# Kernel optimization log

Measured on AMD Instinct MI355X. Metric: run time of the kernel, lower is better.

The kernel has to match this reference:

```python
import jax, jax.numpy as jnp
import numpy as np

N = 8192
F_IN = 1024
F_OUT = 512

def glorot(key, shape):
    limit = np.sqrt(6.0 / (shape[0] + shape[1]))
    return jax.random.uniform(key, shape, minval=-limit, maxval=limit, dtype=jnp.float32)

def setup_inputs() -> dict:
    key = jax.random.key(0)
    k1, k2, k3 = jax.random.split(key, 3)
    x = jax.random.normal(k1, (N, F_IN), dtype=jnp.float32)
    adj = jax.random.uniform(k2, (N, N), dtype=jnp.float32)  # dense nonnegative adjacency
    W = glorot(k3, (F_IN, F_OUT))
    b = jnp.zeros((F_OUT,), dtype=jnp.float32)
    return {"x": x, "adj": adj, "W": W, "b": b}

def reference(x, adj, W, b):
    # GCN layer: relu( D^{-1/2} (A + I) D^{-1/2} @ (x @ W) + b )
    n = adj.shape[0]
    A = adj + jnp.eye(n, dtype=adj.dtype)            # add self loops (tf.diag(In))
    d = jnp.sum(A, axis=1)                            # row-sum degrees
    d_is = d ** -0.5                                  # D^{-1/2}
    # D1 @ A @ D1 expressed as row/col scaling (identical math, no diag GEMMs)
    A_norm = A * d_is[:, None] * d_is[None, :]
    pre_sup = x @ W                                   # [N, F_OUT]
    out = A_norm @ pre_sup + b                        # propagation + bias
    return jax.nn.relu(out)
```

## Files before the change

kernel.cpp:

```cpp
#include <hip/hip_runtime.h>
#include <stdint.h>

#define NN 8192
#define FIN 1024
#define FOUT 512

typedef __attribute__((ext_vector_type(4))) float f32x4;
typedef __attribute__((ext_vector_type(8))) short s16x8;
typedef __attribute__((ext_vector_type(4))) unsigned short u16x4;

__device__ __forceinline__ short f2bf(float f) {
    return __builtin_bit_cast(short, static_cast<__bf16>(f));
}
__device__ __forceinline__ float bf2f(short s) {
    return (float)__builtin_bit_cast(__bf16, s);
}

__global__ __launch_bounds__(256) void prep_kernel(const float* __restrict__ adj,
                                                   short* __restrict__ adjB,
                                                   float* __restrict__ d_is,
                                                   const float* __restrict__ x,
                                                   short* __restrict__ xB,
                                                   const float* __restrict__ W,
                                                   short* __restrict__ WT) {
    __shared__ float red[4];
    __shared__ float T[64][68];
    const int b = blockIdx.x;
    const int t = threadIdx.x;
    if (b < NN) {
        const int row = b;
        const float4* a = reinterpret_cast<const float4*>(adj + (size_t)row * NN);
        u16x4* ob = reinterpret_cast<u16x4*>(adjB + (size_t)row * NN);
        float s = 0.f;
        #pragma unroll 2
        for (int j = t; j < NN / 4; j += 256) {
            float4 v = a[j];
            s += (v.x + v.y) + (v.z + v.w);
            u16x4 p;
            p[0] = (unsigned short)f2bf(v.x); p[1] = (unsigned short)f2bf(v.y);
            p[2] = (unsigned short)f2bf(v.z); p[3] = (unsigned short)f2bf(v.w);
            ob[j] = p;
        }
        #pragma unroll
        for (int off = 32; off > 0; off >>= 1) s += __shfl_down(s, off, 64);
        if ((t & 63) == 0) red[t >> 6] = s;
        __syncthreads();
        if (t == 0) {
            const float d = red[0] + red[1] + red[2] + red[3] + 1.0f;
            d_is[row] = 1.0f / sqrtf(d);
        }
    } else if (b < NN + 4096) {
        const size_t i = ((size_t)(b - NN) * 256 + t) * 8;
        const float4 v0 = *reinterpret_cast<const float4*>(&x[i]);
        const float4 v1 = *reinterpret_cast<const float4*>(&x[i + 4]);
        s16x8 o;
        o[0] = f2bf(v0.x); o[1] = f2bf(v0.y); o[2] = f2bf(v0.z); o[3] = f2bf(v0.w);
        o[4] = f2bf(v1.x); o[5] = f2bf(v1.y); o[6] = f2bf(v1.z); o[7] = f2bf(v1.w);
        *reinterpret_cast<s16x8*>(&xB[i]) = o;
    } else {
        const int bid = b - NN - 4096;
        const int wc = bid & 7;
        const int wk = bid >> 3;
        const int cc = (t & 15) * 4;
        #pragma unroll
        for (int i = 0; i < 4; ++i) {
            const int rr = (t >> 4) + i * 16;
            *reinterpret_cast<float4*>(&T[rr][cc]) =
                *reinterpret_cast<const float4*>(&W[(size_t)(wk * 64 + rr) * FOUT + wc * 64 + cc]);
        }
        __syncthreads();
        const int a = t >> 2;
        const int b0 = (t & 3) * 16;
        s16x8 v0, v1;
        #pragma unroll
        for (int e = 0; e < 8; ++e) { v0[e] = f2bf(T[b0 + e][a]); v1[e] = f2bf(T[b0 + 8 + e][a]); }
        short* dst = &WT[(size_t)(wc * 64 + a) * FIN + wk * 64 + b0];
        *reinterpret_cast<s16x8*>(dst) = v0;
        *reinterpret_cast<s16x8*>(dst + 8) = v1;
    }
}

__global__ __launch_bounds__(256) void rowsum_kernel(const float* __restrict__ adj,
                                                     float* __restrict__ d_is) {
    const int row = blockIdx.x;
    const float4* a = reinterpret_cast<const float4*>(adj + (size_t)row * NN);
    float s = 0.f;
    #pragma unroll 4
    for (int j = threadIdx.x; j < NN / 4; j += 256) {
        float4 v = a[j];
        s += (v.x + v.y) + (v.z + v.w);
    }
    #pragma unroll
    for (int off = 32; off > 0; off >>= 1) s += __shfl_down(s, off, 64);
    __shared__ float red[4];
    if ((threadIdx.x & 63) == 0) red[threadIdx.x >> 6] = s;
    __syncthreads();
    if (threadIdx.x == 0) {
        const float d = red[0] + red[1] + red[2] + red[3] + 1.0f;
        d_is[row] = 1.0f / sqrtf(d);
    }
}

__global__ __launch_bounds__(256) void wt_kernel(const float* __restrict__ W,
                                                 short* __restrict__ WT) {
    __shared__ float T[64][68];
    const int wc = blockIdx.x;
    const int wk = blockIdx.y;
    const int t = threadIdx.x;
    const int cc = (t & 15) * 4;
    #pragma unroll
    for (int i = 0; i < 4; ++i) {
        const int rr = (t >> 4) + i * 16;
        *reinterpret_cast<float4*>(&T[rr][cc]) =
            *reinterpret_cast<const float4*>(&W[(size_t)(wk * 64 + rr) * FOUT + wc * 64 + cc]);
    }
    __syncthreads();
    const int a = t >> 2;
    const int b0 = (t & 3) * 16;
    s16x8 v0, v1;
    #pragma unroll
    for (int e = 0; e < 8; ++e) { v0[e] = f2bf(T[b0 + e][a]); v1[e] = f2bf(T[b0 + 8 + e][a]); }
    short* dst = &WT[(size_t)(wc * 64 + a) * FIN + wk * 64 + b0];
    *reinterpret_cast<s16x8*>(dst) = v0;
    *reinterpret_cast<s16x8*>(dst + 8) = v1;
}

__global__ __launch_bounds__(256, 4) void xwg_kernel(const short* __restrict__ xB,
                                                     const short* __restrict__ WT,
                                                     const float* __restrict__ d_is,
                                                     short* __restrict__ psT) {
    constexpr int NT = FIN / 32;
    __shared__ short As[2][4096];
    __shared__ short Bs[2][2048];

    const int tid = threadIdx.x;
    const int lin = blockIdx.x;
    const int swz = (lin & 7) * 64 + (lin >> 3);
    const int col0 = (swz & 7) * 64;
    const int row0 = (swz >> 3) * 128;

    const int lane = tid & 63;
    const int wv = tid >> 6;
    const int wr = wv >> 1, wc = wv & 1;
    const int l15 = lane & 15;
    const int kq = lane >> 4;
    const int xorv = (l15 & 12) << 2;

    int arow[2], acoff[2];
    #pragma unroll
    for (int i = 0; i < 2; ++i) {
        const int slot = i * 256 + tid;
        const int P = (slot << 4) ^ (slot & 48);
        arow[i] = P >> 6;
        acoff[i] = (P & 63) >> 1;
    }
    const short* Ab = xB + (size_t)row0 * FIN;
    const short* Bb = WT + (size_t)col0 * FIN;

    auto stage = [&](int buf, int k0) {
        #pragma unroll
        for (int i = 0; i < 2; ++i) {
            const short* src = Ab + (size_t)arow[i] * FIN + k0 + acoff[i];
            short* dst = &As[buf][(i * 256 + (tid & 192)) * 8];
            __builtin_amdgcn_global_load_lds(
                (const __attribute__((address_space(1))) unsigned int*)src,
                (__attribute__((address_space(3))) unsigned int*)dst, 16, 0, 0);
        }
        {
            const short* src = Bb + (size_t)arow[0] * FIN + k0 + acoff[0];
            short* dst = &Bs[buf][(tid & 192) * 8];
            __builtin_amdgcn_global_load_lds(
                (const __attribute__((address_space(1))) unsigned int*)src,
                (__attribute__((address_space(3))) unsigned int*)dst, 16, 0, 0);
        }
    };

    f32x4 acc[4][2] = {};
    auto compute = [&](int buf) {
        s16x8 af[4], bfr[2];
        #pragma unroll
        for (int m = 0; m < 4; ++m) {
            const int byteoff = ((wr * 64 + m * 16 + l15) * 64 + kq * 16) ^ xorv;
            af[m] = *reinterpret_cast<const s16x8*>(&As[buf][byteoff >> 1]);
        }
        #pragma unroll
        for (int n = 0; n < 2; ++n) {
            const int byteoff = ((wc * 32 + n * 16 + l15) * 64 + kq * 16) ^ xorv;
            bfr[n] = *reinterpret_cast<const s16x8*>(&Bs[buf][byteoff >> 1]);
        }
        #pragma unroll
        for (int m = 0; m < 4; ++m)
            #pragma unroll
            for (int n = 0; n < 2; ++n)
                acc[m][n] = __builtin_amdgcn_mfma_f32_16x16x32_bf16(af[m], bfr[n], acc[m][n], 0, 0, 0);
    };

    stage(0, 0);
    stage(1, 32);
    int cur = 0;
    #pragma unroll 1
    for (int t = 0; t < NT; ++t) {
        if (t < NT - 1) {
            asm volatile("s_waitcnt vmcnt(3)" ::: "memory");
        } else {
            asm volatile("s_waitcnt vmcnt(0)" ::: "memory");
        }
        __builtin_amdgcn_s_barrier();
        compute(cur);
        if (t + 2 < NT) {
            __builtin_amdgcn_s_barrier();
            stage(cur, (t + 2) * 32);
        }
        cur ^= 1;
    }

    #pragma unroll
    for (int m = 0; m < 4; ++m) {
        const int rbase = row0 + wr * 64 + m * 16 + kq * 4;
        float dr[4];
        #pragma unroll
        for (int j = 0; j < 4; ++j) dr[j] = d_is[rbase + j];
        #pragma unroll
        for (int n = 0; n < 2; ++n) {
            const int col = col0 + wc * 32 + n * 16 + l15;
            u16x4 pk;
            #pragma unroll
            for (int j = 0; j < 4; ++j) pk[j] = (unsigned short)f2bf(dr[j] * acc[m][n][j]);
            *reinterpret_cast<u16x4*>(&psT[(size_t)col * NN + rbase]) = pk;
        }
    }
}

__global__ __launch_bounds__(512, 1) void prop3_kernel(
    const short* __restrict__ adjB, const short* __restrict__ psT,
    short* __restrict__ Pb0, short* __restrict__ Pb1,
    short* __restrict__ Pb2, short* __restrict__ Pb3) {
    extern __shared__ short L[];

    const int tid = threadIdx.x;
    const int lin = blockIdx.x;
    const int swz = (lin & 7) * 32 + (lin >> 3);
    const int col0 = (swz & 1) * 256;
    const int ks = (swz >> 1) & 3;
    const int row0 = (swz >> 3) * 256;

    const int lane = tid & 63;
    const int wv = tid >> 6;
    const int wr = wv >> 2;
    const int wc = wv & 3;
    const int l15 = lane & 15;
    const int kq = lane >> 4;
    const int xorv = (l15 & 12) << 2;

    int srow[2], scol[2];
    #pragma unroll
    for (int i = 0; i < 2; ++i) {
        const int slot = i * 512 + tid;
        const int P = (slot << 4) ^ (slot & 48);
        srow[i] = P >> 6;
        scol[i] = (P & 63) >> 1;
    }
    const size_t kbase = (size_t)ks * 2048;
    const short* Ab = adjB + (size_t)row0 * NN + kbase;
    const short* Bb = psT + (size_t)col0 * NN + kbase;

    auto stageH = [&](int buf, int op, int kh, int t) {
        const short* s0 = op ? Bb : Ab;
        const int k0 = t * 64 + kh * 32;
        short* base = &L[buf * 32768 + op * 16384 + kh * 8192];
        #pragma unroll
        for (int i = 0; i < 2; ++i) {
            const short* src = s0 + (size_t)srow[i] * NN + k0 + scol[i];
            short* dst = base + (i * 512 + (tid & 448)) * 8;
            __builtin_amdgcn_global_load_lds(
                (const __attribute__((address_space(1))) unsigned int*)src,
                (__attribute__((address_space(3))) unsigned int*)dst, 16, 0, 0);
        }
    };

    f32x4 acc[8][4] = {};

#define LDFRAG(BASE, ROW) \
    (*reinterpret_cast<const s16x8*>(&(BASE)[((((ROW) * 64 + kq * 16)) ^ xorv) >> 1]))

#define PHASE(BUF, KH, QM, STAGE_STMT, VM_STMT)                                     \
    do {                                                                            \
        const short* Ah_ = &L[(BUF) * 32768 + (KH) * 8192];                         \
        const short* Bh_ = &L[(BUF) * 32768 + 16384 + (KH) * 8192];                 \
        s16x8 af_[4], bg_[4];                                                       \
        _Pragma("unroll")                                                           \
        for (int m = 0; m < 4; ++m)                                                 \
            af_[m] = LDFRAG(Ah_, wr * 128 + (QM) * 64 + m * 16 + l15);              \
        _Pragma("unroll")                                                           \
        for (int n = 0; n < 4; ++n)                                                 \
            bg_[n] = LDFRAG(Bh_, wc * 64 + n * 16 + l15);                           \
        STAGE_STMT;                                                                 \
        asm volatile("" ::: "memory");                                              \
        __builtin_amdgcn_s_barrier();                                               \
        __builtin_amdgcn_s_setprio(1);                                              \
        _Pragma("unroll")                                                           \
        for (int m = 0; m < 4; ++m)                                                 \
            _Pragma("unroll")                                                       \
            for (int n = 0; n < 4; ++n)                                             \
                acc[(QM) * 4 + m][n] = __builtin_amdgcn_mfma_f32_16x16x32_bf16(     \
                    af_[m], bg_[n], acc[(QM) * 4 + m][n], 0, 0, 0);                 \
        __builtin_amdgcn_s_setprio(0);                                              \
        VM_STMT;                                                                    \
        asm volatile("" ::: "memory");                                              \
        __builtin_amdgcn_s_barrier();                                               \
    } while (0)

#define VM4 asm volatile("s_waitcnt vmcnt(4)" ::: "memory")
#define VM0 asm volatile("s_waitcnt vmcnt(0)" ::: "memory")

    stageH(0, 0, 0, 0); stageH(0, 1, 0, 0);
    stageH(0, 0, 1, 0); stageH(0, 1, 1, 0);
    stageH(1, 0, 0, 1); stageH(1, 1, 0, 1);
    asm volatile("s_waitcnt vmcnt(8)" ::: "memory");
    __builtin_amdgcn_s_barrier();

    PHASE(0, 0, 0, (void)0,             (void)0);
    PHASE(0, 0, 1, (void)0,             VM4);
    PHASE(0, 1, 0, stageH(1, 0, 1, 1),  (void)0);
    PHASE(0, 1, 1, stageH(1, 1, 1, 1),  VM4);

    #pragma unroll 1
    for (int t = 1; t <= 30; ++t) {
        const int buf = t & 1, nb = buf ^ 1, tn = t + 1;
        PHASE(buf, 0, 0, stageH(nb, 0, 0, tn), (void)0);
        PHASE(buf, 0, 1, stageH(nb, 1, 0, tn), VM4);
        PHASE(buf, 1, 0, stageH(nb, 0, 1, tn), (void)0);
        PHASE(buf, 1, 1, stageH(nb, 1, 1, tn), VM4);
    }

    PHASE(1, 0, 0, (void)0, (void)0);
    PHASE(1, 0, 1, (void)0, VM0);
    PHASE(1, 1, 0, (void)0, (void)0);
    PHASE(1, 1, 1, (void)0, (void)0);

    {
        short* Pt = (ks == 0) ? Pb0 : (ks == 1) ? Pb1 : (ks == 2) ? Pb2 : Pb3;
        #pragma unroll
        for (int mi = 0; mi < 8; ++mi) {
            const int rbase = row0 + wr * 128 + mi * 16 + kq * 4;
            #pragma unroll
            for (int n = 0; n < 4; ++n) {
                const int col = col0 + wc * 64 + n * 16 + l15;
                #pragma unroll
                for (int j = 0; j < 4; ++j)
                    Pt[(size_t)(rbase + j) * FOUT + col] = f2bf(acc[mi][n][j]);
            }
        }
    }
#undef PHASE
#undef LDFRAG
#undef VM4
#undef VM0
}

__global__ __launch_bounds__(256) void ep4_kernel(
    const short* __restrict__ Pb0, const short* __restrict__ Pb1,
    const short* __restrict__ Pb2, const short* __restrict__ Pb3,
    float* __restrict__ out,
    const short* __restrict__ psT, const float* __restrict__ d_is,
    const float* __restrict__ bias) {
    const int col0 = blockIdx.x * 128;
    const int row0 = blockIdx.y * 32;
    const int t = threadIdx.x;
    const int c = col0 + (t & 31) * 4;
    const float4 bb = *reinterpret_cast<const float4*>(&bias[c]);
    #pragma unroll
    for (int it = 0; it < 4; ++it) {
        const int r = row0 + (t >> 5) + it * 8;
        const size_t idx = (size_t)r * FOUT + c;
        const u16x4 a = *reinterpret_cast<const u16x4*>(&Pb0[idx]);
        const u16x4 b4 = *reinterpret_cast<const u16x4*>(&Pb1[idx]);
        const u16x4 c4 = *reinterpret_cast<const u16x4*>(&Pb2[idx]);
        const u16x4 d4 = *reinterpret_cast<const u16x4*>(&Pb3[idx]);
        const float dr = d_is[r];
        float s[4], o4[4];
        #pragma unroll
        for (int j = 0; j < 4; ++j) s[j] = bf2f(psT[(size_t)(c + j) * NN + r]);
        const float bbv[4] = {bb.x, bb.y, bb.z, bb.w};
        #pragma unroll
        for (int j = 0; j < 4; ++j) {
            const float sum = ((bf2f((short)a[j]) + bf2f((short)b4[j])) +
                               (bf2f((short)c4[j]) + bf2f((short)d4[j]))) + s[j];
            o4[j] = fmaxf(dr * sum + bbv[j], 0.f);
        }
        float4 o = {o4[0], o4[1], o4[2], o4[3]};
        *reinterpret_cast<float4*>(&out[idx]) = o;
    }
}

template<int KLEN, int MODE>
__global__ __launch_bounds__(256, 4) void gemm_kernel(
    const float* __restrict__ A, const short* __restrict__ B,
    const float* __restrict__ d_is,
    short* __restrict__ psT,
    float* __restrict__ P0, float* __restrict__ P1) {
    constexpr int KS = (MODE == 1) ? 2 : 1;
    constexpr int Ksub = KLEN / KS;
    constexpr int NT = Ksub / 32;
    constexpr int LDA = 40;
    __shared__ short As[2][128 * LDA];
    __shared__ short Bs[2][64 * LDA];

    const int tid = threadIdx.x;
    const int nchunk = gridDim.x >> 3;
    const int lin = blockIdx.x;
    const int swz = (lin & 7) * nchunk + (lin >> 3);
    const int col0 = (swz & 7) * 64;
    const int yp = (swz >> 3) & 63;
    const int ks = swz >> 9;
    const int row0 = yp * 128;
    const int kbase = ks * Ksub;

    const int lane = tid & 63;
    const int wv = tid >> 6;
    const int wr = wv >> 1, wc = wv & 1;
    const int l15 = lane & 15;
    const int koff = (lane >> 4) * 8;

    const int ar = tid >> 1, ak = (tid & 1) * 16;
    const float* Abase = A + (size_t)(row0 + ar) * KLEN + kbase + ak;
    const int br = tid >> 2, bk = (tid & 3) * 8;
    const short* Bbase = B + (size_t)(col0 + br) * KLEN + kbase + bk;

    float4 qa0, qa1, qa2, qa3;
    s16x8 qb;
    auto loadG = [&](int k0) {
        const float4* p = reinterpret_cast<const float4*>(Abase + k0);
        qa0 = p[0]; qa1 = p[1]; qa2 = p[2]; qa3 = p[3];
        qb = *reinterpret_cast<const s16x8*>(Bbase + k0);
    };
    auto writeL = [&](int buf) {
        const float a[16] = {qa0.x, qa0.y, qa0.z, qa0.w, qa1.x, qa1.y, qa1.z, qa1.w,
                             qa2.x, qa2.y, qa2.z, qa2.w, qa3.x, qa3.y, qa3.z, qa3.w};
        s16x8 v0, v1;
        #pragma unroll
        for (int e = 0; e < 8; ++e) { v0[e] = f2bf(a[e]); v1[e] = f2bf(a[8 + e]); }
        *reinterpret_cast<s16x8*>(&As[buf][ar * LDA + ak]) = v0;
        *reinterpret_cast<s16x8*>(&As[buf][ar * LDA + ak + 8]) = v1;
        *reinterpret_cast<s16x8*>(&Bs[buf][br * LDA + bk]) = qb;
    };

    f32x4 acc[4][2] = {};
    auto compute = [&](int buf) {
        s16x8 af[4], bfr[2];
        #pragma unroll
        for (int m = 0; m < 4; ++m)
            af[m] = *reinterpret_cast<const s16x8*>(&As[buf][(wr * 64 + m * 16 + l15) * LDA + koff]);
        #pragma unroll
        for (int n = 0; n < 2; ++n)
            bfr[n] = *reinterpret_cast<const s16x8*>(&Bs[buf][(wc * 32 + n * 16 + l15) * LDA + koff]);
        #pragma unroll
        for (int m = 0; m < 4; ++m)
            #pragma unroll
            for (int n = 0; n < 2; ++n)
                acc[m][n] = __builtin_amdgcn_mfma_f32_16x16x32_bf16(af[m], bfr[n], acc[m][n], 0, 0, 0);
    };

    loadG(0);
    writeL(0);
    __syncthreads();
    int cur = 0;
    for (int t = 0; t < NT; ++t) {
        if (t + 1 < NT) loadG((t + 1) * 32);
        compute(cur);
        if (t + 1 < NT) writeL(cur ^ 1);
        __syncthreads();
        cur ^= 1;
    }

    if (MODE == 0) {
        #pragma unroll
        for (int m = 0; m < 4; ++m) {
            const int rbase = row0 + wr * 64 + m * 16 + (lane >> 4) * 4;
            float dr[4];
            #pragma unroll
            for (int j = 0; j < 4; ++j) dr[j] = d_is[rbase + j];
            #pragma unroll
            for (int n = 0; n < 2; ++n) {
                const int col = col0 + wc * 32 + n * 16 + l15;
                u16x4 pk;
                #pragma unroll
                for (int j = 0; j < 4; ++j) pk[j] = (unsigned short)f2bf(dr[j] * acc[m][n][j]);
                *reinterpret_cast<u16x4*>(&psT[(size_t)col * NN + rbase]) = pk;
            }
        }
    } else {
        float* tgt = (ks == 0) ? P0 : P1;
        #pragma unroll
        for (int m = 0; m < 4; ++m) {
            const int rbase = row0 + wr * 64 + m * 16 + (lane >> 4) * 4;
            #pragma unroll
            for (int n = 0; n < 2; ++n) {
                const int col = col0 + wc * 32 + n * 16 + l15;
                f32x4 v = acc[m][n];
                if (ks == 0) {
                    const u16x4 sv = *reinterpret_cast<const u16x4*>(&psT[(size_t)col * NN + rbase]);
                    #pragma unroll
                    for (int j = 0; j < 4; ++j) v[j] += bf2f((short)sv[j]);
                }
                #pragma unroll
                for (int j = 0; j < 4; ++j)
                    tgt[(size_t)(rbase + j) * FOUT + col] = v[j];
            }
        }
    }
}

__global__ __launch_bounds__(256) void ep_kernel(const float* __restrict__ P0,
                                                 float* __restrict__ out,
                                                 const float* __restrict__ d_is,
                                                 const float* __restrict__ bias) {
    const size_t idx = ((size_t)blockIdx.x * 256 + threadIdx.x) * 4;
    const int row = (int)(idx >> 9);
    const int col = (int)(idx & 511);
    const float4 p0 = *reinterpret_cast<const float4*>(&P0[idx]);
    const float4 p1 = *reinterpret_cast<const float4*>(&out[idx]);
    const float4 bb = *reinterpret_cast<const float4*>(&bias[col]);
    const float dr = d_is[row];
    float4 o;
    o.x = fmaxf(dr * (p0.x + p1.x) + bb.x, 0.f);
    o.y = fmaxf(dr * (p0.y + p1.y) + bb.y, 0.f);
    o.z = fmaxf(dr * (p0.z + p1.z) + bb.z, 0.f);
    o.w = fmaxf(dr * (p0.w + p1.w) + bb.w, 0.f);
    *reinterpret_cast<float4*>(&out[idx]) = o;
}

extern "C" void kernel_launch(void* const* d_in, const int* in_sizes, int n_in,
                              void* d_out, int out_size, void* d_ws, size_t ws_size,
                              hipStream_t stream) {
    const float* x   = (const float*)d_in[0];
    const float* adj = (const float*)d_in[1];
    const float* W   = (const float*)d_in[2];
    const float* b   = (const float*)d_in[3];
    float* out = (float*)d_out;

    const size_t NEED = (size_t)FOUT * NN * 2 + (size_t)FOUT * FIN * 2
                      + (size_t)NN * FIN * 2 + 4ull * NN * FOUT * 2
                      + NN * 4 + (size_t)NN * NN * 2;

    if (ws_size >= NEED) {
        short* psT = (short*)d_ws;
        short* WT  = psT + (size_t)FOUT * NN;
        short* xB  = WT + (size_t)FOUT * FIN;
        short* Pb0 = xB + (size_t)NN * FIN;
        short* Pb1 = Pb0 + (size_t)NN * FOUT;
        short* Pb2 = Pb1 + (size_t)NN * FOUT;
        short* Pb3 = Pb2 + (size_t)NN * FOUT;
        float* dis = (float*)(Pb3 + (size_t)NN * FOUT);
        short* adjB = (short*)(dis + NN);

        hipLaunchKernelGGL(prep_kernel, dim3(NN + 4096 + 128), dim3(256), 0, stream,
                           adj, adjB, dis, x, xB, W, WT);
        hipLaunchKernelGGL(xwg_kernel, dim3(512), dim3(256), 0, stream, xB, WT, dis, psT);
        hipLaunchKernelGGL(prop3_kernel, dim3(256), dim3(512), 131072, stream,
                           adjB, psT, Pb0, Pb1, Pb2, Pb3);
        hipLaunchKernelGGL(ep4_kernel, dim3(4, 256), dim3(256), 0, stream,
                           Pb0, Pb1, Pb2, Pb3, out, psT, dis, b);
    } else {
        short* psT = (short*)d_ws;
        short* WT  = psT + (size_t)FOUT * NN;
        float* P0  = (float*)(WT + (size_t)FOUT * FIN);
        float* dis = P0 + (size_t)NN * FOUT;

        hipLaunchKernelGGL(rowsum_kernel, dim3(NN), dim3(256), 0, stream, adj, dis);
        hipLaunchKernelGGL(wt_kernel, dim3(8, 16), dim3(256), 0, stream, W, WT);
        hipLaunchKernelGGL((gemm_kernel<FIN, 0>), dim3(512), dim3(256), 0, stream,
                           x, WT, dis, psT, nullptr, nullptr);
        hipLaunchKernelGGL((gemm_kernel<NN, 1>), dim3(1024), dim3(256), 0, stream,
                           adj, psT, dis, psT, P0, out);
        hipLaunchKernelGGL(ep_kernel, dim3(NN * FOUT / 1024), dim3(256), 0, stream,
                           P0, out, dis, b);
    }
}
```

Measured before the change: 192.1 us.

## Convert fp32 adjacency to bf16 inside propagation GEMM instead of materializing adjB

After: 244.5 us. 1.27x slower.

```diff
diff --git a/kernel.cpp b/kernel.cpp
--- a/kernel.cpp
+++ b/kernel.cpp
@@ -17,7 +17,6 @@
 }
 
 __global__ __launch_bounds__(256) void prep_kernel(const float* __restrict__ adj,
-                                                   short* __restrict__ adjB,
                                                    float* __restrict__ d_is,
                                                    const float* __restrict__ x,
                                                    short* __restrict__ xB,
@@ -30,16 +29,11 @@
     if (b < NN) {
         const int row = b;
         const float4* a = reinterpret_cast<const float4*>(adj + (size_t)row * NN);
-        u16x4* ob = reinterpret_cast<u16x4*>(adjB + (size_t)row * NN);
         float s = 0.f;
-        #pragma unroll 2
+        #pragma unroll 4
         for (int j = t; j < NN / 4; j += 256) {
             float4 v = a[j];
             s += (v.x + v.y) + (v.z + v.w);
-            u16x4 p;
-            p[0] = (unsigned short)f2bf(v.x); p[1] = (unsigned short)f2bf(v.y);
-            p[2] = (unsigned short)f2bf(v.z); p[3] = (unsigned short)f2bf(v.w);
-            ob[j] = p;
         }
         #pragma unroll
         for (int off = 32; off > 0; off >>= 1) s += __shfl_down(s, off, 64);
@@ -231,8 +225,8 @@
     }
 }
 
-__global__ __launch_bounds__(512, 1) void prop3_kernel(
-    const short* __restrict__ adjB, const short* __restrict__ psT,
+__global__ __launch_bounds__(512, 1) void prop4_kernel(
+    const float* __restrict__ adj, const short* __restrict__ psT,
     short* __restrict__ Pb0, short* __restrict__ Pb1,
     short* __restrict__ Pb2, short* __restrict__ Pb3) {
     extern __shared__ short L[];
@@ -261,20 +255,44 @@
         scol[i] = (P & 63) >> 1;
     }
     const size_t kbase = (size_t)ks * 2048;
-    const short* Ab = adjB + (size_t)row0 * NN + kbase;
     const short* Bb = psT + (size_t)col0 * NN + kbase;
 
-    auto stageH = [&](int buf, int op, int kh, int t) {
-        const short* s0 = op ? Bb : Ab;
+    auto stageB = [&](int buf, int kh, int t) {
         const int k0 = t * 64 + kh * 32;
-        short* base = &L[buf * 32768 + op * 16384 + kh * 8192];
+        short* base = &L[buf * 32768 + 16384 + kh * 8192];
         #pragma unroll
         for (int i = 0; i < 2; ++i) {
-            const short* src = s0 + (size_t)srow[i] * NN + k0 + scol[i];
+            const short* src = Bb + (size_t)srow[i] * NN + k0 + scol[i];
             short* dst = base + (i * 512 + (tid & 448)) * 8;
             __builtin_amdgcn_global_load_lds(
                 (const __attribute__((address_space(1))) unsigned int*)src,
                 (__attribute__((address_space(3))) unsigned int*)dst, 16, 0, 0);
+        }
+    };
+
+    const int ar = tid & 255;
+    const int akh = tid >> 8;
+    const float* Abase = adj + (size_t)(row0 + ar) * NN + kbase + akh * 32;
+    const int axr = (ar >> 2) & 3;
+    float4 qa0, qa1, qa2, qa3, qa4, qa5, qa6, qa7;
+
+    auto loadA = [&](int t) {
+        const float4* p = reinterpret_cast<const float4*>(Abase + t * 64);
+        qa0 = p[0]; qa1 = p[1]; qa2 = p[2]; qa3 = p[3];
+        qa4 = p[4]; qa5 = p[5]; qa6 = p[6]; qa7 = p[7];
+    };
+    auto writeA = [&](int buf) {
+        short* base = &L[buf * 32768 + akh * 8192 + ar * 32];
+        const float fa[32] = {qa0.x, qa0.y, qa0.z, qa0.w, qa1.x, qa1.y, qa1.z, qa1.w,
+                              qa2.x, qa2.y, qa2.z, qa2.w, qa3.x, qa3.y, qa3.z, qa3.w,
+                              qa4.x, qa4.y, qa4.z, qa4.w, qa5.x, qa5.y, qa5.z, qa5.w,
+                              qa6.x, qa6.y, qa6.z, qa6.w, qa7.x, qa7.y, qa7.z, qa7.w};
+        #pragma unroll
+        for (int c = 0; c < 4; ++c) {
+            s16x8 v;
+            #pragma unroll
+            for (int e = 0; e < 8; ++e) v[e] = f2bf(fa[c * 8 + e]);
+            *reinterpret_cast<s16x8*>(base + (c ^ axr) * 8) = v;
         }
     };
 
@@ -310,27 +328,37 @@
         __builtin_amdgcn_s_barrier();                                               \
     } while (0)
 
-#define VM4 asm volatile("s_waitcnt vmcnt(4)" ::: "memory")
-#define VM0 asm volatile("s_waitcnt vmcnt(0)" ::: "memory")
-
-    stageH(0, 0, 0, 0); stageH(0, 1, 0, 0);
-    stageH(0, 0, 1, 0); stageH(0, 1, 1, 0);
-    stageH(1, 0, 0, 1); stageH(1, 1, 0, 1);
-    asm volatile("s_waitcnt vmcnt(8)" ::: "memory");
+#define WRITEA(NB)                                                                  \
+    do { writeA(NB);                                                                \
+         asm volatile("s_waitcnt lgkmcnt(0)" ::: "memory");                         \
+         __builtin_amdgcn_sched_barrier(0); } while (0)
+
+#define VM10 asm volatile("s_waitcnt vmcnt(10)" ::: "memory")
+#define VM2  asm volatile("s_waitcnt vmcnt(2)" ::: "memory")
+#define VM0  asm volatile("s_waitcnt vmcnt(0)" ::: "memory")
+
+    loadA(0);
+    writeA(0);
+    asm volatile("s_waitcnt lgkmcnt(0)" ::: "memory");
+    __builtin_amdgcn_sched_barrier(0);
+    stageB(0, 0, 0); stageB(0, 1, 0);
+    loadA(1);
+    stageB(1, 0, 1);
+    asm volatile("s_waitcnt vmcnt(12)" ::: "memory");
     __builtin_amdgcn_s_barrier();
 
-    PHASE(0, 0, 0, (void)0,             (void)0);
-    PHASE(0, 0, 1, (void)0,             VM4);
-    PHASE(0, 1, 0, stageH(1, 0, 1, 1),  (void)0);
-    PHASE(0, 1, 1, stageH(1, 1, 1, 1),  VM4);
+    PHASE(0, 0, 0, (void)0,           (void)0);
+    PHASE(0, 0, 1, (void)0,           VM10);
+    PHASE(0, 1, 0, WRITEA(1),         (void)0);
+    PHASE(0, 1, 1, stageB(1, 1, 1),   VM2);
 
     #pragma unroll 1
     for (int t = 1; t <= 30; ++t) {
         const int buf = t & 1, nb = buf ^ 1, tn = t + 1;
-        PHASE(buf, 0, 0, stageH(nb, 0, 0, tn), (void)0);
-        PHASE(buf, 0, 1, stageH(nb, 1, 0, tn), VM4);
-        PHASE(buf, 1, 0, stageH(nb, 0, 1, tn), (void)0);
-        PHASE(buf, 1, 1, stageH(nb, 1, 1, tn), VM4);
+        PHASE(buf, 0, 0, loadA(tn),           (void)0);
+        PHASE(buf, 0, 1, stageB(nb, 0, tn),   VM10);
+        PHASE(buf, 1, 0, WRITEA(nb),          (void)0);
+        PHASE(buf, 1, 1, stageB(nb, 1, tn),   VM2);
     }
 
     PHASE(1, 0, 0, (void)0, (void)0);
@@ -338,24 +366,25 @@
     PHASE(1, 1, 0, (void)0, (void)0);
     PHASE(1, 1, 1, (void)0, (void)0);
 
-    {
-        short* Pt = (ks == 0) ? Pb0 : (ks == 1) ? Pb1 : (ks == 2) ? Pb2 : Pb3;
-        #pragma unroll
-        for (int mi = 0; mi < 8; ++mi) {
-            const int rbase = row0 + wr * 128 + mi * 16 + kq * 4;
-            #pragma unroll
-            for (int n = 0; n < 4; ++n) {
-                const int col = col0 + wc * 64 + n * 16 + l15;
-                #pragma unroll
-                for (int j = 0; j < 4; ++j)
-                    Pt[(size_t)(rbase + j) * FOUT + col] = f2bf(acc[mi][n][j]);
-            }
-        }
-    }
 #undef PHASE
 #undef LDFRAG
-#undef VM4
+#undef WRITEA
+#undef VM10
+#undef VM2
 #undef VM0
+
+    short* Pt = (ks == 0) ? Pb0 : (ks == 1) ? Pb1 : (ks == 2) ? Pb2 : Pb3;
+    #pragma unroll
+    for (int mi = 0; mi < 8; ++mi) {
+        const int rbase = row0 + wr * 128 + mi * 16 + kq * 4;
+        #pragma unroll
+        for (int n = 0; n < 4; ++n) {
+            const int col = col0 + wc * 64 + n * 16 + l15;
+            #pragma unroll
+            for (int j = 0; j < 4; ++j)
+                Pt[(size_t)(rbase + j) * FOUT + col] = f2bf(acc[mi][n][j]);
+        }
+    }
 }
 
 __global__ __launch_bounds__(256) void ep4_kernel(
@@ -540,8 +569,7 @@
     float* out = (float*)d_out;
 
     const size_t NEED = (size_t)FOUT * NN * 2 + (size_t)FOUT * FIN * 2
-                      + (size_t)NN * FIN * 2 + 4ull * NN * FOUT * 2
-                      + NN * 4 + (size_t)NN * NN * 2;
+                      + (size_t)NN * FIN * 2 + 4ull * NN * FOUT * 2 + NN * 4;
 
     if (ws_size >= NEED) {
         short* psT = (short*)d_ws;
@@ -552,13 +580,12 @@
         short* Pb2 = Pb1 + (size_t)NN * FOUT;
         short* Pb3 = Pb2 + (size_t)NN * FOUT;
         float* dis = (float*)(Pb3 + (size_t)NN * FOUT);
-        short* adjB = (short*)(dis + NN);
 
         hipLaunchKernelGGL(prep_kernel, dim3(NN + 4096 + 128), dim3(256), 0, stream,
-                           adj, adjB, dis, x, xB, W, WT);
+                           adj, dis, x, xB, W, WT);
         hipLaunchKernelGGL(xwg_kernel, dim3(512), dim3(256), 0, stream, xB, WT, dis, psT);
-        hipLaunchKernelGGL(prop3_kernel, dim3(256), dim3(512), 131072, stream,
-                           adjB, psT, Pb0, Pb1, Pb2, Pb3);
+        hipLaunchKernelGGL(prop4_kernel, dim3(256), dim3(512), 131072, stream,
+                           adj, psT, Pb0, Pb1, Pb2, Pb3);
         hipLaunchKernelGGL(ep4_kernel, dim3(4, 256), dim3(256), 0, stream,
                            Pb0, Pb1, Pb2, Pb3, out, psT, dis, b);
     } else {
```

## Load propagation B operand directly to registers and halve LDS staging

Applied to the files above, without the earlier changes.

After: 263.7 us. 37.3% more time.

```diff
diff --git a/kernel.cpp b/kernel.cpp
--- a/kernel.cpp
+++ b/kernel.cpp
@@ -231,18 +231,19 @@
     }
 }
 
-__global__ __launch_bounds__(512, 1) void prop3_kernel(
+__global__ __launch_bounds__(512, 2) void prop3b_kernel(
     const short* __restrict__ adjB, const short* __restrict__ psT,
     short* __restrict__ Pb0, short* __restrict__ Pb1,
     short* __restrict__ Pb2, short* __restrict__ Pb3) {
     extern __shared__ short L[];
+    constexpr int NT = 32;
 
     const int tid = threadIdx.x;
     const int lin = blockIdx.x;
     const int swz = (lin & 7) * 32 + (lin >> 3);
     const int col0 = (swz & 1) * 256;
-    const int ks = (swz >> 1) & 3;
-    const int row0 = (swz >> 3) * 256;
+    const int row0 = ((swz >> 1) & 31) * 256;
+    const int ks = (swz >> 6) & 3;
 
     const int lane = tid & 63;
     const int wv = tid >> 6;
@@ -262,15 +263,14 @@
     }
     const size_t kbase = (size_t)ks * 2048;
     const short* Ab = adjB + (size_t)row0 * NN + kbase;
-    const short* Bb = psT + (size_t)col0 * NN + kbase;
-
-    auto stageH = [&](int buf, int op, int kh, int t) {
-        const short* s0 = op ? Bb : Ab;
+    const short* Bp = psT + (size_t)(col0 + wc * 64 + l15) * NN + kbase + kq * 8;
+
+    auto stageA = [&](int buf, int kh, int t) {
         const int k0 = t * 64 + kh * 32;
-        short* base = &L[buf * 32768 + op * 16384 + kh * 8192];
+        short* base = &L[buf * 16384 + kh * 8192];
         #pragma unroll
         for (int i = 0; i < 2; ++i) {
-            const short* src = s0 + (size_t)srow[i] * NN + k0 + scol[i];
+            const short* src = Ab + (size_t)srow[i] * NN + k0 + scol[i];
             short* dst = base + (i * 512 + (tid & 448)) * 8;
             __builtin_amdgcn_global_load_lds(
                 (const __attribute__((address_space(1))) unsigned int*)src,
@@ -280,82 +280,85 @@
 
     f32x4 acc[8][4] = {};
 
-#define LDFRAG(BASE, ROW) \
-    (*reinterpret_cast<const s16x8*>(&(BASE)[((((ROW) * 64 + kq * 16)) ^ xorv) >> 1]))
-
-#define PHASE(BUF, KH, QM, STAGE_STMT, VM_STMT)                                     \
+#define FENCE asm volatile("" ::: "memory")
+
+#define LOADB(B, T)                                                                 \
     do {                                                                            \
-        const short* Ah_ = &L[(BUF) * 32768 + (KH) * 8192];                         \
-        const short* Bh_ = &L[(BUF) * 32768 + 16384 + (KH) * 8192];                 \
-        s16x8 af_[4], bg_[4];                                                       \
         _Pragma("unroll")                                                           \
-        for (int m = 0; m < 4; ++m)                                                 \
-            af_[m] = LDFRAG(Ah_, wr * 128 + (QM) * 64 + m * 16 + l15);              \
+        for (int kh_ = 0; kh_ < 2; ++kh_)                                           \
+            _Pragma("unroll")                                                       \
+            for (int n_ = 0; n_ < 4; ++n_)                                          \
+                B[kh_][n_] = *reinterpret_cast<const s16x8*>(                       \
+                    Bp + (size_t)n_ * 16 * NN + (T) * 64 + kh_ * 32);               \
+        FENCE;                                                                      \
+    } while (0)
+
+#define COMPUTE(BUF, B)                                                             \
+    do {                                                                            \
         _Pragma("unroll")                                                           \
-        for (int n = 0; n < 4; ++n)                                                 \
-            bg_[n] = LDFRAG(Bh_, wc * 64 + n * 16 + l15);                           \
-        STAGE_STMT;                                                                 \
-        asm volatile("" ::: "memory");                                              \
+        for (int kh_ = 0; kh_ < 2; ++kh_) {                                         \
+            const short* Ah_ = &L[(BUF) * 16384 + kh_ * 8192];                      \
+            s16x8 af_[8];                                                           \
+            _Pragma("unroll")                                                       \
+            for (int m_ = 0; m_ < 8; ++m_) {                                        \
+                const int ROW = wr * 128 + m_ * 16 + l15;                           \
+                af_[m_] = *reinterpret_cast<const s16x8*>(                          \
+                    &Ah_[((ROW * 64 + kq * 16) ^ xorv) >> 1]);                      \
+            }                                                                       \
+            __builtin_amdgcn_s_setprio(1);                                          \
+            _Pragma("unroll")                                                       \
+            for (int m_ = 0; m_ < 8; ++m_)                                          \
+                _Pragma("unroll")                                                   \
+                for (int n_ = 0; n_ < 4; ++n_)                                      \
+                    acc[m_][n_] = __builtin_amdgcn_mfma_f32_16x16x32_bf16(          \
+                        af_[m_], B[kh_][n_], acc[m_][n_], 0, 0, 0);                 \
+            __builtin_amdgcn_s_setprio(0);                                          \
+        }                                                                           \
+    } while (0)
+
+#define ITER(T, BCUR, BNXT)                                                         \
+    do {                                                                            \
+        if ((T) < NT - 1) { asm volatile("s_waitcnt vmcnt(12)" ::: "memory"); }     \
+        else              { asm volatile("s_waitcnt vmcnt(8)"  ::: "memory"); }     \
         __builtin_amdgcn_s_barrier();                                               \
-        __builtin_amdgcn_s_setprio(1);                                              \
-        _Pragma("unroll")                                                           \
-        for (int m = 0; m < 4; ++m)                                                 \
-            _Pragma("unroll")                                                       \
-            for (int n = 0; n < 4; ++n)                                             \
-                acc[(QM) * 4 + m][n] = __builtin_amdgcn_mfma_f32_16x16x32_bf16(     \
-                    af_[m], bg_[n], acc[(QM) * 4 + m][n], 0, 0, 0);                 \
-        __builtin_amdgcn_s_setprio(0);                                              \
-        VM_STMT;                                                                    \
-        asm volatile("" ::: "memory");                                              \
+        FENCE;                                                                      \
+        COMPUTE((T) & 1, BCUR);                                                     \
+        FENCE;                                                                      \
         __builtin_amdgcn_s_barrier();                                               \
+        if ((T) + 1 < NT) LOADB(BNXT, (T) + 1);                                     \
+        if ((T) + 2 < NT) { stageA((T) & 1, 0, (T) + 2);                            \
+                            stageA((T) & 1, 1, (T) + 2); FENCE; }                   \
     } while (0)
 
-#define VM4 asm volatile("s_waitcnt vmcnt(4)" ::: "memory")
-#define VM0 asm volatile("s_waitcnt vmcnt(0)" ::: "memory")
-
-    stageH(0, 0, 0, 0); stageH(0, 1, 0, 0);
-    stageH(0, 0, 1, 0); stageH(0, 1, 1, 0);
-    stageH(1, 0, 0, 1); stageH(1, 1, 0, 1);
-    asm volatile("s_waitcnt vmcnt(8)" ::: "memory");
-    __builtin_amdgcn_s_barrier();
-
-    PHASE(0, 0, 0, (void)0,             (void)0);
-    PHASE(0, 0, 1, (void)0,             VM4);
-    PHASE(0, 1, 0, stageH(1, 0, 1, 1),  (void)0);
-    PHASE(0, 1, 1, stageH(1, 1, 1, 1),  VM4);
+    s16x8 bA[2][4], bB[2][4];
+
+    stageA(0, 0, 0); stageA(0, 1, 0); FENCE;
+    LOADB(bA, 0);
+    stageA(1, 0, 1); stageA(1, 1, 1); FENCE;
 
     #pragma unroll 1
-    for (int t = 1; t <= 30; ++t) {
-        const int buf = t & 1, nb = buf ^ 1, tn = t + 1;
-        PHASE(buf, 0, 0, stageH(nb, 0, 0, tn), (void)0);
-        PHASE(buf, 0, 1, stageH(nb, 1, 0, tn), VM4);
-        PHASE(buf, 1, 0, stageH(nb, 0, 1, tn), (void)0);
-        PHASE(buf, 1, 1, stageH(nb, 1, 1, tn), VM4);
-    }
-
-    PHASE(1, 0, 0, (void)0, (void)0);
-    PHASE(1, 0, 1, (void)0, VM0);
-    PHASE(1, 1, 0, (void)0, (void)0);
-    PHASE(1, 1, 1, (void)0, (void)0);
-
-    {
-        short* Pt = (ks == 0) ? Pb0 : (ks == 1) ? Pb1 : (ks == 2) ? Pb2 : Pb3;
-        #pragma unroll
-        for (int mi = 0; mi < 8; ++mi) {
-            const int rbase = row0 + wr * 128 + mi * 16 + kq * 4;
-            #pragma unroll
-            for (int n = 0; n < 4; ++n) {
-                const int col = col0 + wc * 64 + n * 16 + l15;
-                #pragma unroll
-                for (int j = 0; j < 4; ++j)
-                    Pt[(size_t)(rbase + j) * FOUT + col] = f2bf(acc[mi][n][j]);
-            }
-        }
-    }
-#undef PHASE
-#undef LDFRAG
-#undef VM4
-#undef VM0
+    for (int tt = 0; tt < NT; tt += 2) {
+        ITER(tt, bA, bB);
+        ITER(tt + 1, bB, bA);
+    }
+
+#undef ITER
+#undef COMPUTE
+#undef LOADB
+#undef FENCE
+
+    short* Pt = (ks == 0) ? Pb0 : (ks == 1) ? Pb1 : (ks == 2) ? Pb2 : Pb3;
+    #pragma unroll
+    for (int mi = 0; mi < 8; ++mi) {
+        const int rbase = row0 + wr * 128 + mi * 16 + kq * 4;
+        #pragma unroll
+        for (int n = 0; n < 4; ++n) {
+            const int col = col0 + wc * 64 + n * 16 + l15;
+            #pragma unroll
+            for (int j = 0; j < 4; ++j)
+                Pt[(size_t)(rbase + j) * FOUT + col] = f2bf(acc[mi][n][j]);
+        }
+    }
 }
 
 __global__ __launch_bounds__(256) void ep4_kernel(
@@ -557,7 +560,7 @@
         hipLaunchKernelGGL(prep_kernel, dim3(NN + 4096 + 128), dim3(256), 0, stream,
                            adj, adjB, dis, x, xB, W, WT);
         hipLaunchKernelGGL(xwg_kernel, dim3(512), dim3(256), 0, stream, xB, WT, dis, psT);
-        hipLaunchKernelGGL(prop3_kernel, dim3(256), dim3(512), 131072, stream,
+        hipLaunchKernelGGL(prop3b_kernel, dim3(256), dim3(512), 65536, stream,
                            adjB, psT, Pb0, Pb1, Pb2, Pb3);
         hipLaunchKernelGGL(ep4_kernel, dim3(4, 256), dim3(256), 0, stream,
                            Pb0, Pb1, Pb2, Pb3, out, psT, dis, b);
```
